# Kernel tuning notes

Measured on AMD Instinct MI355X. Metric: run time of the kernel, lower is better.

## Reference

```python
import jax, jax.numpy as jnp
import numpy as np

NUM_AGENTS = 64
IN_FEATURES = 512
OUT_FEATURES = 512
BATCH = 2048


def setup_inputs() -> dict:
    key = jax.random.key(0)
    k1, k2, k3, k4 = jax.random.split(key, 4)
    which_agents = jax.random.randint(k1, (BATCH,), 0, NUM_AGENTS, dtype=jnp.int64 if jax.config.jax_enable_x64 else jnp.int32)
    x = jax.random.normal(k2, (BATCH, IN_FEATURES), dtype=jnp.float32)
    # kaiming_uniform_(a=sqrt(5)) -> bound = sqrt(6 / ((1 + 5) * fan_in)) = 1/sqrt(fan_in)
    bound_w = 1.0 / np.sqrt(IN_FEATURES)
    weight = jax.random.uniform(k3, (NUM_AGENTS, OUT_FEATURES, IN_FEATURES), jnp.float32, -bound_w, bound_w)
    bound_b = 1.0 / np.sqrt(IN_FEATURES)
    bias = jax.random.uniform(k4, (NUM_AGENTS, OUT_FEATURES), jnp.float32, -bound_b, bound_b)
    return {"which_agents": which_agents, "input": x, "weight": weight, "bias": bias}


def reference(which_agents, input, weight, bias):
    # weight[which_agents]: [B, out, in]; batched matvec with input [B, in]
    w = weight[which_agents]          # [B, O, I]
    b = bias[which_agents]            # [B, O]
    return jnp.einsum('boi,bi->bo', w, input) + b
```

## Files before the change

### kernel.cpp

```cpp
#include <hip/hip_runtime.h>


constexpr int BATCH  = 2048;
constexpr int NAGENT = 64;
constexpr int IN_F   = 512;
constexpr int OUT_F  = 512;

constexpr int BN  = 128;
constexpr int MCH = 64;
constexpr int XS  = IN_F + 8;

typedef __attribute__((ext_vector_type(8))) short short8;
typedef __attribute__((ext_vector_type(4))) float f32x4;
typedef __attribute__((ext_vector_type(4))) unsigned int u32x4;
typedef __bf16 bf16x2 __attribute__((ext_vector_type(2)));

__device__ inline unsigned pk_bf(float lo, float hi) {
  bf16x2 v;
  v[0] = (__bf16)lo;
  v[1] = (__bf16)hi;
  return __builtin_bit_cast(unsigned, v);
}

__global__ __launch_bounds__(1024, 4) void agent_linear_mfma4(
    const int*   __restrict__ which,
    const float* __restrict__ x,
    const float* __restrict__ weight,
    const float* __restrict__ bias,
    float*       __restrict__ out) {
  const int tid   = threadIdx.x;
  const int lane  = tid & 63;
  const int wid   = tid >> 6;
  const int w8    = wid & 7;
  const int kh    = wid >> 3;

  const int bid   = blockIdx.x;
  const int agent = (bid & 7) | ((bid >> 5) << 3);
  const int obase = ((bid >> 3) & 3) * BN;

  __shared__ int rowlist_s[BATCH];
  __shared__ int wsum_s[16];
  __shared__ __align__(16) unsigned short Xs[MCH * XS];
  __shared__ float Rs[8][MCH][17];

  const int nl = lane & 15;
  const int kq = lane >> 4;

  const float* wp = weight + ((size_t)(agent * OUT_F + obase + w8 * 16 + nl)) * IN_F
                  + kh * 256 + kq * 8;

  float4 pa[3], pb[3];
#pragma unroll
  for (int j = 0; j < 3; ++j) {
    pa[j] = *(const float4*)(wp + j * 32);
    pb[j] = *(const float4*)(wp + j * 32 + 4);
  }

  const float bv = bias[agent * OUT_F + obase + w8 * 16 + nl];

  int2 v = ((const int2*)which)[tid];
  int lc = (v.x == agent) + (v.y == agent);
  int s = lc;
#pragma unroll
  for (int off = 1; off < 64; off <<= 1) {
    int t = __shfl_up(s, off);
    if (lane >= off) s += t;
  }
  if (lane == 63) wsum_s[wid] = s;
  __syncthreads();
  int base = 0, count = 0;
#pragma unroll
  for (int w = 0; w < 16; ++w) {
    int ws = wsum_s[w];
    if (w < wid) base += ws;
    count += ws;
  }
  {
    int pos = base + s - lc;
    if (v.x == agent) rowlist_s[pos++] = 2 * tid;
    if (v.y == agent) rowlist_s[pos]   = 2 * tid + 1;
  }
  __syncthreads();

  for (int m0 = 0; m0 < count; m0 += MCH) {
    const int mcount = min(MCH, count - m0);
    const int nfrag  = (mcount + 15) >> 4;

#pragma unroll
    for (int t = 0; t < 8; ++t) {
      int idx = t * 1024 + tid;
      int r   = idx >> 7;
      int c4  = idx & 127;
      if (r < mcount) {
        float4 xv = *(const float4*)(x + (size_t)rowlist_s[m0 + r] * IN_F + c4 * 4);
        uint2 w2;
        w2.x = pk_bf(xv.x, xv.y);
        w2.y = pk_bf(xv.z, xv.w);
        *(uint2*)&Xs[r * XS + c4 * 4] = w2;
      }
    }
    __syncthreads();

    f32x4 acc[4] = {{0.f,0.f,0.f,0.f},{0.f,0.f,0.f,0.f},
                    {0.f,0.f,0.f,0.f},{0.f,0.f,0.f,0.f}};
    const int kbase = kh * 256;
#pragma unroll
    for (int k = 0; k < 8; ++k) {
      float4 c0 = pa[k % 3], c1 = pb[k % 3];
      if (k + 3 < 8) {
        pa[k % 3] = *(const float4*)(wp + (k + 3) * 32);
        pb[k % 3] = *(const float4*)(wp + (k + 3) * 32 + 4);
      }
      u32x4 q;
      q[0] = pk_bf(c0.x, c0.y); q[1] = pk_bf(c0.z, c0.w);
      q[2] = pk_bf(c1.x, c1.y); q[3] = pk_bf(c1.z, c1.w);
      short8 bfr = __builtin_bit_cast(short8, q);
#pragma unroll
      for (int i = 0; i < 4; ++i) {
        if (i < nfrag) {
          short8 af = *(const short8*)&Xs[(i * 16 + nl) * XS + kbase + k * 32 + kq * 8];
          acc[i] = __builtin_amdgcn_mfma_f32_16x16x32_bf16(af, bfr, acc[i], 0, 0, 0);
        }
      }
    }

    if (kh == 1) {
#pragma unroll
      for (int i = 0; i < 4; ++i)
        if (i < nfrag)
#pragma unroll
          for (int r = 0; r < 4; ++r)
            Rs[w8][i * 16 + kq * 4 + r][nl] = acc[i][r];
    }
    __syncthreads();

    if (kh == 0) {
#pragma unroll
      for (int i = 0; i < 4; ++i) {
        if (i < nfrag) {
#pragma unroll
          for (int r = 0; r < 4; ++r) {
            int m = i * 16 + kq * 4 + r;
            if (m < mcount) {
              out[(size_t)rowlist_s[m0 + m] * OUT_F + obase + w8 * 16 + nl] =
                  acc[i][r] + Rs[w8][m][nl] + bv;
            }
          }
        }
      }
    }

    if (m0 + MCH < count) {
#pragma unroll
      for (int j = 0; j < 3; ++j) {
        pa[j] = *(const float4*)(wp + j * 32);
        pb[j] = *(const float4*)(wp + j * 32 + 4);
      }
    }
  }
}

extern "C" void kernel_launch(void* const* d_in, const int* in_sizes, int n_in,
                              void* d_out, int out_size, void* d_ws, size_t ws_size,
                              hipStream_t stream) {
  const int*   which = (const int*)d_in[0];
  const float* x     = (const float*)d_in[1];
  const float* w     = (const float*)d_in[2];
  const float* b     = (const float*)d_in[3];
  float*       out   = (float*)d_out;

  dim3 grid(OUT_F / BN * NAGENT);
  agent_linear_mfma4<<<grid, dim3(1024), 0, stream>>>(which, x, w, b, out);
}
```

Baseline: 104.4 us.

## Split K across blocks with atomic accumulation instead of in-block reduction

The two K halves now run in separate 512-thread blocks, so the grid doubles to 512 blocks. Each block gathers only its half of the x rows and adds its partial result into out with atomicAdd, after a memset zeroes the output. This removes the shared-memory reduction buffer and its extra barrier, and gives more, smaller blocks to spread across CUs. The cost is an extra memset, twice the routing-list scans, and float atomics on every output, which also makes the summation order nondeterministic.

```diff
diff --git a/kernel.cpp b/kernel.cpp
--- a/kernel.cpp
+++ b/kernel.cpp
@@ -7,8 +7,9 @@
 constexpr int OUT_F  = 512;
 
 constexpr int BN  = 128;
+constexpr int KH  = 256;
 constexpr int MCH = 64;
-constexpr int XS  = IN_F + 8;
+constexpr int XS2 = KH + 8;
 
 typedef __attribute__((ext_vector_type(8))) short short8;
 typedef __attribute__((ext_vector_type(4))) float f32x4;
@@ -22,32 +23,35 @@
   return __builtin_bit_cast(unsigned, v);
 }
 
-__global__ __launch_bounds__(1024, 4) void agent_linear_mfma4(
+__global__ __launch_bounds__(512, 4) void agent_linear_mfma9(
     const int*   __restrict__ which,
     const float* __restrict__ x,
     const float* __restrict__ weight,
     const float* __restrict__ bias,
     float*       __restrict__ out) {
-  const int tid   = threadIdx.x;
-  const int lane  = tid & 63;
-  const int wid   = tid >> 6;
-  const int w8    = wid & 7;
-  const int kh    = wid >> 3;
+  const int tid  = threadIdx.x;
+  const int lane = tid & 63;
+  const int wid  = tid >> 6;
 
   const int bid   = blockIdx.x;
-  const int agent = (bid & 7) | ((bid >> 5) << 3);
-  const int obase = ((bid >> 3) & 3) * BN;
+  const int agent = (bid & 7) | ((bid >> 6) << 3);
+  const int sel   = (bid >> 3) & 7;
+  const int nt    = sel & 3;
+  const int khb   = sel >> 2;
+  const int obase = nt * BN;
+  const int kbase = khb * KH;
 
+  __shared__ int wsum_s[8];
   __shared__ int rowlist_s[BATCH];
-  __shared__ int wsum_s[16];
-  __shared__ __align__(16) unsigned short Xs[MCH * XS];
-  __shared__ float Rs[8][MCH][17];
+  __shared__ __align__(16) unsigned short Xs[MCH * XS2];
+
+  const int4 v = ((const int4*)which)[tid];
 
   const int nl = lane & 15;
   const int kq = lane >> 4;
 
-  const float* wp = weight + ((size_t)(agent * OUT_F + obase + w8 * 16 + nl)) * IN_F
-                  + kh * 256 + kq * 8;
+  const float* wp = weight + ((size_t)(agent * OUT_F + obase + wid * 16 + nl)) * IN_F
+                  + kbase + kq * 8;
 
   float4 pa[3], pb[3];
 #pragma unroll
@@ -56,10 +60,11 @@
     pb[j] = *(const float4*)(wp + j * 32 + 4);
   }
 
-  const float bv = bias[agent * OUT_F + obase + w8 * 16 + nl];
+  const float bv = bias[agent * OUT_F + obase + wid * 16 + nl];
 
-  int2 v = ((const int2*)which)[tid];
-  int lc = (v.x == agent) + (v.y == agent);
+  int m0_ = (v.x == agent), m1_ = (v.y == agent),
+      m2_ = (v.z == agent), m3_ = (v.w == agent);
+  int lc = m0_ + m1_ + m2_ + m3_;
   int s = lc;
 #pragma unroll
   for (int off = 1; off < 64; off <<= 1) {
@@ -70,40 +75,44 @@
   __syncthreads();
   int base = 0, count = 0;
 #pragma unroll
-  for (int w = 0; w < 16; ++w) {
+  for (int w = 0; w < 8; ++w) {
     int ws = wsum_s[w];
     if (w < wid) base += ws;
     count += ws;
   }
   {
     int pos = base + s - lc;
-    if (v.x == agent) rowlist_s[pos++] = 2 * tid;
-    if (v.y == agent) rowlist_s[pos]   = 2 * tid + 1;
+    int i0 = 4 * tid;
+    if (m0_) rowlist_s[pos++] = i0;
+    if (m1_) rowlist_s[pos++] = i0 + 1;
+    if (m2_) rowlist_s[pos++] = i0 + 2;
+    if (m3_) rowlist_s[pos]   = i0 + 3;
   }
-  __syncthreads();
 
   for (int m0 = 0; m0 < count; m0 += MCH) {
     const int mcount = min(MCH, count - m0);
     const int nfrag  = (mcount + 15) >> 4;
 
+    __syncthreads();
+
 #pragma unroll
     for (int t = 0; t < 8; ++t) {
-      int idx = t * 1024 + tid;
-      int r   = idx >> 7;
-      int c4  = idx & 127;
+      int idx = t * 512 + tid;
+      int r   = idx >> 6;
+      int c4  = idx & 63;
       if (r < mcount) {
-        float4 xv = *(const float4*)(x + (size_t)rowlist_s[m0 + r] * IN_F + c4 * 4);
+        float4 xv = *(const float4*)(x + (size_t)rowlist_s[m0 + r] * IN_F
+                                       + kbase + c4 * 4);
         uint2 w2;
         w2.x = pk_bf(xv.x, xv.y);
         w2.y = pk_bf(xv.z, xv.w);
-        *(uint2*)&Xs[r * XS + c4 * 4] = w2;
+        *(uint2*)&Xs[r * XS2 + c4 * 4] = w2;
       }
     }
     __syncthreads();
 
     f32x4 acc[4] = {{0.f,0.f,0.f,0.f},{0.f,0.f,0.f,0.f},
                     {0.f,0.f,0.f,0.f},{0.f,0.f,0.f,0.f}};
-    const int kbase = kh * 256;
 #pragma unroll
     for (int k = 0; k < 8; ++k) {
       float4 c0 = pa[k % 3], c1 = pb[k % 3];
@@ -118,33 +127,22 @@
 #pragma unroll
       for (int i = 0; i < 4; ++i) {
         if (i < nfrag) {
-          short8 af = *(const short8*)&Xs[(i * 16 + nl) * XS + kbase + k * 32 + kq * 8];
+          short8 af = *(const short8*)&Xs[(i * 16 + nl) * XS2 + k * 32 + kq * 8];
           acc[i] = __builtin_amdgcn_mfma_f32_16x16x32_bf16(af, bfr, acc[i], 0, 0, 0);
         }
       }
     }
 
-    if (kh == 1) {
+    const float badd = (khb == 0) ? bv : 0.f;
 #pragma unroll
-      for (int i = 0; i < 4; ++i)
-        if (i < nfrag)
+    for (int i = 0; i < 4; ++i) {
+      if (i < nfrag) {
 #pragma unroll
-          for (int r = 0; r < 4; ++r)
-            Rs[w8][i * 16 + kq * 4 + r][nl] = acc[i][r];
-    }
-    __syncthreads();
-
-    if (kh == 0) {
-#pragma unroll
-      for (int i = 0; i < 4; ++i) {
-        if (i < nfrag) {
-#pragma unroll
-          for (int r = 0; r < 4; ++r) {
-            int m = i * 16 + kq * 4 + r;
-            if (m < mcount) {
-              out[(size_t)rowlist_s[m0 + m] * OUT_F + obase + w8 * 16 + nl] =
-                  acc[i][r] + Rs[w8][m][nl] + bv;
-            }
+        for (int r = 0; r < 4; ++r) {
+          int m = i * 16 + kq * 4 + r;
+          if (m < mcount) {
+            atomicAdd(&out[(size_t)rowlist_s[m0 + m] * OUT_F + obase + wid * 16 + nl],
+                      acc[i][r] + badd);
           }
         }
       }
@@ -169,6 +167,8 @@
   const float* b     = (const float*)d_in[3];
   float*       out   = (float*)d_out;
 
-  dim3 grid(OUT_F / BN * NAGENT);
-  agent_linear_mfma4<<<grid, dim3(1024), 0, stream>>>(which, x, w, b, out);
+  hipMemsetAsync(d_out, 0, out_size, stream);
+
+  dim3 grid(4 * 2 * NAGENT);
+  agent_linear_mfma9<<<grid, dim3(512), 0, stream>>>(which, x, w, b, out);
 }
```

Measured after the change: 108.9 us. +4.4%, slower.
